# Kernel optimization log

Measured on AMD Instinct MI355X. Metric: run time of the kernel, lower is better.

Reference implementation:

```python
import jax, jax.numpy as jnp
import numpy as np

N, E, D_IN, H, D = 170000, 1200000, 128, 4, 32
NEG_SLOPE = 0.2


def setup_inputs() -> dict:
    key = jax.random.key(0)
    ks = jax.random.split(key, 8)
    x = jax.random.normal(ks[0], (N, D_IN), dtype=jnp.float32)
    # xavier-normal-ish scale for linear weights
    W_embed = jax.random.normal(ks[1], (D_IN, H * D), dtype=jnp.float32) * (2.0 / (D_IN + H * D)) ** 0.5
    a_src = jax.random.normal(ks[2], (H, D), dtype=jnp.float32) * (2.0 / (1 + H * D)) ** 0.5
    a_dst = jax.random.normal(ks[3], (H, D), dtype=jnp.float32) * (2.0 / (1 + H * D)) ** 0.5
    W_lin = jax.random.normal(ks[4], (D_IN, H * D), dtype=jnp.float32) * (2.0 / (D_IN + H * D)) ** 0.5
    bias = jnp.zeros((H * D,), dtype=jnp.float32)
    src = jax.random.randint(ks[5], (E,), 0, N, dtype=jnp.int32)
    dst = jax.random.randint(ks[6], (E,), 0, N, dtype=jnp.int32)
    return {"x": x, "W_embed": W_embed, "a_src": a_src, "a_dst": a_dst,
            "W_lin": W_lin, "bias": bias, "src": src, "dst": dst}


def reference(x, W_embed, a_src, a_dst, W_lin, bias, src, dst):
    n = x.shape[0]
    # node projections: [N, H, D]
    h = (x @ W_embed).reshape(n, H, D)
    dot_src = jnp.einsum('nhd,hd->nh', h, a_src)  # [N, H]
    dot_dst = jnp.einsum('nhd,hd->nh', h, a_dst)  # [N, H]
    # edge attention logits: leaky_relu(dot_src[u] + dot_dst[v])  [E, H]
    z = dot_src[src] + dot_dst[dst]
    logit = jnp.where(z >= 0, z, NEG_SLOPE * z)
    # edge softmax over incoming edges of each destination node
    m = jax.ops.segment_max(logit, dst, num_segments=n)          # [N, H]
    e = jnp.exp(logit - m[dst])                                   # [E, H]
    denom = jax.ops.segment_sum(e, dst, num_segments=n)          # [N, H]
    prob = e / denom[dst]                                         # [E, H]
    # weighted scatter-sum aggregation: sum_e prob_e * h[src_e]
    msg = h[src] * prob[:, :, None]                               # [E, H, D]
    out = jax.ops.segment_sum(msg, dst, num_segments=n)          # [N, H, D]
    out = out.reshape(n, H * D)
    out = out + x @ W_lin
    out = out + bias[None, :]
    return out
```

## Files before the change

kernel.cpp:

```cpp
#include <hip/hip_runtime.h>
#include <hip/hip_bf16.h>

static constexpr int   N_NODES   = 170000;
static constexpr int   E_EDGES   = 1200000;
static constexpr float NEG_SLOPE = 0.2f;

typedef __attribute__((ext_vector_type(8))) short bfrag8;
typedef __attribute__((ext_vector_type(4))) float facc4;

__device__ __forceinline__ short f2bf(float f) {
    __hip_bfloat16 h = __float2bfloat16(f);
    return *reinterpret_cast<short*>(&h);
}

__global__ void wt_init_kernel(const float* __restrict__ We,
                               const float* __restrict__ Wl,
                               const float* __restrict__ a_src,
                               const float* __restrict__ a_dst,
                               short* __restrict__ WtG,
                               int* __restrict__ deg)
{
    const int t = threadIdx.x;
    if (blockIdx.x < 128) {
        const int k = blockIdx.x;
        if (t < 128) WtG[t * 128 + k] = f2bf(We[k * 128 + t]);
        else         WtG[t * 128 + k] = f2bf(Wl[k * 128 + (t - 128)]);
    } else if (blockIdx.x < 136) {
        const int idx = (blockIdx.x - 128) * 256 + t;
        if (idx < 1024) {
            const int g = idx >> 7;
            const int k = idx & 127;
            const int hh = g & 3;
            const float* av = (g < 4) ? a_src : a_dst;
            float s = 0.f;
            #pragma unroll
            for (int d = 0; d < 32; ++d)
                s += We[k * 128 + hh * 32 + d] * av[hh * 32 + d];
            WtG[(256 + g) * 128 + k] = f2bf(s);
        } else {
            const int z = idx - 1024;
            WtG[(264 + (z >> 7)) * 128 + (z & 127)] = 0;
        }
    }
    const int i = blockIdx.x * 256 + t;
    if (i < N_NODES) deg[i] = 0;
}

__global__ void hist_kernel(const int* __restrict__ dst,
                            int* __restrict__ deg,
                            int* __restrict__ seq)
{
    int e = blockIdx.x * blockDim.x + threadIdx.x;
    if (e < E_EDGES) {
        const int s = atomicAdd(&deg[dst[e]], 1);
        __builtin_nontemporal_store(s, &seq[e]);
    }
}

__global__ __launch_bounds__(256) void scan_local_kernel(
    const int* __restrict__ deg, int* __restrict__ row_ptr, int* __restrict__ bsum)
{
    __shared__ int sh[256];
    const int t = threadIdx.x;
    const int base = blockIdx.x * 1024 + t * 4;
    int v0 = (base + 0 < N_NODES) ? deg[base + 0] : 0;
    int v1 = (base + 1 < N_NODES) ? deg[base + 1] : 0;
    int v2 = (base + 2 < N_NODES) ? deg[base + 2] : 0;
    int v3 = (base + 3 < N_NODES) ? deg[base + 3] : 0;
    const int tot = v0 + v1 + v2 + v3;
    sh[t] = tot;
    __syncthreads();
    for (int off = 1; off < 256; off <<= 1) {
        int add = (t >= off) ? sh[t - off] : 0;
        __syncthreads();
        sh[t] += add;
        __syncthreads();
    }
    const int excl = sh[t] - tot;
    if (base + 0 < N_NODES) row_ptr[base + 0] = excl;
    if (base + 1 < N_NODES) row_ptr[base + 1] = excl + v0;
    if (base + 2 < N_NODES) row_ptr[base + 2] = excl + v0 + v1;
    if (base + 3 < N_NODES) row_ptr[base + 3] = excl + v0 + v1 + v2;
    if (t == 255) bsum[blockIdx.x] = sh[255];
}

__global__ __launch_bounds__(256) void scan_block_kernel(
    const int* __restrict__ bsum, int* __restrict__ boff, int nblk)
{
    __shared__ int sh[256];
    const int t = threadIdx.x;
    const int v = (t < nblk) ? bsum[t] : 0;
    sh[t] = v;
    __syncthreads();
    for (int off = 1; off < 256; off <<= 1) {
        int add = (t >= off) ? sh[t - off] : 0;
        __syncthreads();
        sh[t] += add;
        __syncthreads();
    }
    boff[t] = sh[t] - v;
}

__global__ void scan_add_kernel(int* __restrict__ row_ptr,
                                const int* __restrict__ boff)
{
    int i = blockIdx.x * blockDim.x + threadIdx.x;
    if (i < N_NODES) row_ptr[i] += boff[i >> 10];
    if (i == 0) row_ptr[N_NODES] = E_EDGES;
}

__global__ void csr_place_kernel(const int* __restrict__ src,
                                 const int* __restrict__ dst,
                                 const int* __restrict__ seq,
                                 const int* __restrict__ rowp,
                                 int* __restrict__ srcs)
{
    int e = blockIdx.x * blockDim.x + threadIdx.x;
    if (e >= E_EDGES) return;
    const int p = rowp[dst[e]] + seq[e];
    __builtin_nontemporal_store(src[e], &srcs[p]);
}

static constexpr int LDB = 136;

__global__ __launch_bounds__(256, 2) void mfma_gemm_kernel(
    const float* __restrict__ x,
    const short* __restrict__ WtG,
    const float* __restrict__ bias,
    short* __restrict__ hbuf,
    float* __restrict__ dsrc,
    float* __restrict__ ddst,
    float* __restrict__ outp)
{
    __shared__ short Bs[272 * LDB];
    const int tid  = threadIdx.x;
    const long row0 = (long)blockIdx.x * 128;

    #pragma unroll
    for (int it = 0; it < 17; ++it) {
        const int idx = it * 256 + tid;
        const int n   = idx >> 4;
        const int kc  = (idx & 15) * 8;
        *(int4*)&Bs[n * LDB + kc] = *(const int4*)&WtG[n * 128 + kc];
    }

    const int w    = tid >> 6;
    const int l    = tid & 63;
    const int col  = l & 15;
    const int quad = l >> 4;

    long ar0 = row0 + w * 32 + col;
    long ar1 = ar0 + 16;
    if (ar0 > N_NODES - 1) ar0 = N_NODES - 1;
    if (ar1 > N_NODES - 1) ar1 = N_NODES - 1;
    const float4* xp0 = (const float4*)&x[ar0 * 128 + quad * 8];
    const float4* xp1 = (const float4*)&x[ar1 * 128 + quad * 8];
    float4 av[2][4][2];
    #pragma unroll
    for (int ks = 0; ks < 4; ++ks) {
        av[0][ks][0] = xp0[ks * 8 + 0];
        av[0][ks][1] = xp0[ks * 8 + 1];
        av[1][ks][0] = xp1[ks * 8 + 0];
        av[1][ks][1] = xp1[ks * 8 + 1];
    }
    bfrag8 afr[2][4];
    #pragma unroll
    for (int m = 0; m < 2; ++m)
        #pragma unroll
        for (int ks = 0; ks < 4; ++ks) {
            bfrag8 t;
            t[0] = f2bf(av[m][ks][0].x); t[1] = f2bf(av[m][ks][0].y);
            t[2] = f2bf(av[m][ks][0].z); t[3] = f2bf(av[m][ks][0].w);
            t[4] = f2bf(av[m][ks][1].x); t[5] = f2bf(av[m][ks][1].y);
            t[6] = f2bf(av[m][ks][1].z); t[7] = f2bf(av[m][ks][1].w);
            afr[m][ks] = t;
        }
    __syncthreads();

    facc4 acc[2][8];
    facc4 adot[2];

    #pragma unroll
    for (int m = 0; m < 2; ++m) {
        adot[m] = (facc4)(0.f);
        #pragma unroll
        for (int t = 0; t < 8; ++t) acc[m][t] = (facc4)(0.f);
    }

    #pragma unroll
    for (int ks = 0; ks < 4; ++ks) {
        #pragma unroll
        for (int t = 0; t < 8; ++t) {
            const bfrag8 b = *(const bfrag8*)&Bs[(t * 16 + col) * LDB + ks * 32 + quad * 8];
            acc[0][t] = __builtin_amdgcn_mfma_f32_16x16x32_bf16(afr[0][ks], b, acc[0][t], 0, 0, 0);
            acc[1][t] = __builtin_amdgcn_mfma_f32_16x16x32_bf16(afr[1][ks], b, acc[1][t], 0, 0, 0);
        }
        const bfrag8 bd = *(const bfrag8*)&Bs[(256 + col) * LDB + ks * 32 + quad * 8];
        adot[0] = __builtin_amdgcn_mfma_f32_16x16x32_bf16(afr[0][ks], bd, adot[0], 0, 0, 0);
        adot[1] = __builtin_amdgcn_mfma_f32_16x16x32_bf16(afr[1][ks], bd, adot[1], 0, 0, 0);
    }

    #pragma unroll
    for (int m = 0; m < 2; ++m) {
        const long rbase = row0 + w * 32 + m * 16 + quad * 4;
        #pragma unroll
        for (int r = 0; r < 4; ++r) {
            const long mm = rbase + r;
            if (mm >= N_NODES) continue;
            #pragma unroll
            for (int t = 0; t < 8; ++t)
                hbuf[mm * 128 + t * 16 + col] = f2bf(acc[m][t][r]);
            if (col < 4)      dsrc[mm * 4 + col]       = adot[m][r];
            else if (col < 8) ddst[mm * 4 + (col - 4)] = adot[m][r];
        }
    }

    #pragma unroll
    for (int m = 0; m < 2; ++m)
        #pragma unroll
        for (int t = 0; t < 8; ++t) acc[m][t] = (facc4)(0.f);

    #pragma unroll
    for (int ks = 0; ks < 4; ++ks) {
        #pragma unroll
        for (int t = 0; t < 8; ++t) {
            const bfrag8 b = *(const bfrag8*)&Bs[(128 + t * 16 + col) * LDB + ks * 32 + quad * 8];
            acc[0][t] = __builtin_amdgcn_mfma_f32_16x16x32_bf16(afr[0][ks], b, acc[0][t], 0, 0, 0);
            acc[1][t] = __builtin_amdgcn_mfma_f32_16x16x32_bf16(afr[1][ks], b, acc[1][t], 0, 0, 0);
        }
    }

    #pragma unroll
    for (int t = 0; t < 8; ++t) {
        const float bv = bias[t * 16 + col];
        #pragma unroll
        for (int m = 0; m < 2; ++m) {
            const long rbase = row0 + w * 32 + m * 16 + quad * 4;
            #pragma unroll
            for (int r = 0; r < 4; ++r) {
                const long mm = rbase + r;
                if (mm < N_NODES) outp[mm * 128 + t * 16 + col] = acc[m][t][r] + bv;
            }
        }
    }
}

__global__ __launch_bounds__(256) void agg_kernel(
    const int* __restrict__ row_ptr, const int* __restrict__ srcs,
    const float* __restrict__ dsrc, const float* __restrict__ ddst,
    const short* __restrict__ hbuf, float* __restrict__ outp)
{
    const long node = (long)blockIdx.x * 4 + (threadIdx.x >> 6);
    if (node >= N_NODES) return;
    const int lane = threadIdx.x & 63;
    const int head = lane >> 4;
    const int c2   = lane << 1;
    const int start = __builtin_amdgcn_readfirstlane(row_ptr[node]);
    const int end   = __builtin_amdgcn_readfirstlane(row_ptr[node + 1]);
    if (start == end) return;

    const float dd = ddst[node * 4 + head];

    float a0 = 0.f, a1 = 0.f, dn = 0.f;

#define EDGE_LOAD(i) \
    const int   s##i = __builtin_amdgcn_readlane(sv, k + i); \
    const float e##i = dsrc[s##i * 4 + head]; \
    const uint  h##i = *(const uint*)&hbuf[(long)s##i * 128 + c2];

#define EDGE_ACC(i) { \
    float z = e##i + dd; \
    z = (z >= 0.f) ? z : NEG_SLOPE * z; \
    float wv = __expf(z); \
    if (k + i >= chunk) wv = 0.f; \
    dn += wv; \
    a0 = fmaf(wv, __uint_as_float(h##i << 16),        a0); \
    a1 = fmaf(wv, __uint_as_float(h##i & 0xFFFF0000u), a1); }

    int j = start;
    while (j < end) {
        const int rem   = end - j;
        const int chunk = rem < 64 ? rem : 64;
        int idx = j + lane;
        if (idx > end - 1) idx = end - 1;
        const int sv = srcs[idx];
        for (int k = 0; k < chunk; k += 8) {
            EDGE_LOAD(0) EDGE_LOAD(1) EDGE_LOAD(2) EDGE_LOAD(3)
            EDGE_LOAD(4) EDGE_LOAD(5) EDGE_LOAD(6) EDGE_LOAD(7)
            EDGE_ACC(0) EDGE_ACC(1) EDGE_ACC(2) EDGE_ACC(3)
            EDGE_ACC(4) EDGE_ACC(5) EDGE_ACC(6) EDGE_ACC(7)
        }
        j += chunk;
    }
#undef EDGE_LOAD
#undef EDGE_ACC

    const float inv = 1.f / dn;
    float2* op = (float2*)&outp[node * 128 + c2];
    float2 o = *op;
    o.x += a0 * inv;
    o.y += a1 * inv;
    *op = o;
}

extern "C" void kernel_launch(void* const* d_in, const int* in_sizes, int n_in,
                              void* d_out, int out_size, void* d_ws, size_t ws_size,
                              hipStream_t stream)
{
    const float* x       = (const float*)d_in[0];
    const float* W_embed = (const float*)d_in[1];
    const float* a_src   = (const float*)d_in[2];
    const float* a_dst   = (const float*)d_in[3];
    const float* W_lin   = (const float*)d_in[4];
    const float* bias    = (const float*)d_in[5];
    const int*   src     = (const int*)d_in[6];
    const int*   dst     = (const int*)d_in[7];
    float* outp = (float*)d_out;

    char* ws = (char*)d_ws;
    short* WtG   = (short*)ws;  ws += (size_t)272 * 128 * sizeof(short);
    short* hbuf  = (short*)ws;  ws += (size_t)N_NODES * 128 * sizeof(short);
    int*   srcs  = (int*)ws;    ws += (size_t)E_EDGES * sizeof(int);
    float* dsrc  = (float*)ws;  ws += (size_t)N_NODES * 4 * sizeof(float);
    float* ddst  = (float*)ws;  ws += (size_t)N_NODES * 4 * sizeof(float);
    int*   deg   = (int*)ws;    ws += (size_t)N_NODES * sizeof(int);
    int*   rowp  = (int*)ws;    ws += (size_t)(N_NODES + 16) * sizeof(int);
    int*   bsum  = (int*)ws;    ws += 256 * sizeof(int);
    int*   boff  = (int*)ws;    ws += 256 * sizeof(int);

    int* seq = (int*)dsrc;

    const int SCAN_BLKS = (N_NODES + 1023) / 1024;

    wt_init_kernel<<<(N_NODES + 255) / 256, 256, 0, stream>>>(
        W_embed, W_lin, a_src, a_dst, WtG, deg);
    hist_kernel<<<(E_EDGES + 255) / 256, 256, 0, stream>>>(dst, deg, seq);
    scan_local_kernel<<<SCAN_BLKS, 256, 0, stream>>>(deg, rowp, bsum);
    scan_block_kernel<<<1, 256, 0, stream>>>(bsum, boff, SCAN_BLKS);
    scan_add_kernel<<<(N_NODES + 255) / 256, 256, 0, stream>>>(rowp, boff);

    csr_place_kernel<<<(E_EDGES + 255) / 256, 256, 0, stream>>>(
        src, dst, seq, rowp, srcs);

    mfma_gemm_kernel<<<(N_NODES + 127) / 128, 256, 0, stream>>>(
        x, WtG, bias, hbuf, dsrc, ddst, outp);

    agg_kernel<<<(N_NODES + 3) / 4, 256, 0, stream>>>(
        rowp, srcs, dsrc, ddst, hbuf, outp);
}
```

Before: 389.7 us.

## Halve GEMM LDS footprint with staged weight loads; precompute edge weights per lane in aggregation

```diff
diff --git a/kernel.cpp b/kernel.cpp
--- a/kernel.cpp
+++ b/kernel.cpp
@@ -123,7 +123,7 @@
 
 static constexpr int LDB = 136;
 
-__global__ __launch_bounds__(256, 2) void mfma_gemm_kernel(
+__global__ __launch_bounds__(256, 4) void mfma_gemm_kernel(
     const float* __restrict__ x,
     const short* __restrict__ WtG,
     const float* __restrict__ bias,
@@ -132,17 +132,9 @@
     float* __restrict__ ddst,
     float* __restrict__ outp)
 {
-    __shared__ short Bs[272 * LDB];
+    __shared__ short Bs[144 * LDB];
     const int tid  = threadIdx.x;
     const long row0 = (long)blockIdx.x * 128;
-
-    #pragma unroll
-    for (int it = 0; it < 17; ++it) {
-        const int idx = it * 256 + tid;
-        const int n   = idx >> 4;
-        const int kc  = (idx & 15) * 8;
-        *(int4*)&Bs[n * LDB + kc] = *(const int4*)&WtG[n * 128 + kc];
-    }
 
     const int w    = tid >> 6;
     const int l    = tid & 63;
@@ -163,6 +155,16 @@
         av[1][ks][0] = xp1[ks * 8 + 0];
         av[1][ks][1] = xp1[ks * 8 + 1];
     }
+
+    #pragma unroll
+    for (int it = 0; it < 9; ++it) {
+        const int idx = it * 256 + tid;
+        const int n   = idx >> 4;
+        const int kc  = (idx & 15) * 8;
+        const int gn  = (n < 128) ? n : (n + 128);
+        *(int4*)&Bs[n * LDB + kc] = *(const int4*)&WtG[gn * 128 + kc];
+    }
+
     bfrag8 afr[2][4];
     #pragma unroll
     for (int m = 0; m < 2; ++m)
@@ -195,7 +197,7 @@
             acc[0][t] = __builtin_amdgcn_mfma_f32_16x16x32_bf16(afr[0][ks], b, acc[0][t], 0, 0, 0);
             acc[1][t] = __builtin_amdgcn_mfma_f32_16x16x32_bf16(afr[1][ks], b, acc[1][t], 0, 0, 0);
         }
-        const bfrag8 bd = *(const bfrag8*)&Bs[(256 + col) * LDB + ks * 32 + quad * 8];
+        const bfrag8 bd = *(const bfrag8*)&Bs[(128 + col) * LDB + ks * 32 + quad * 8];
         adot[0] = __builtin_amdgcn_mfma_f32_16x16x32_bf16(afr[0][ks], bd, adot[0], 0, 0, 0);
         adot[1] = __builtin_amdgcn_mfma_f32_16x16x32_bf16(afr[1][ks], bd, adot[1], 0, 0, 0);
     }
@@ -215,6 +217,16 @@
         }
     }
 
+    __syncthreads();
+    #pragma unroll
+    for (int it = 0; it < 8; ++it) {
+        const int idx = it * 256 + tid;
+        const int n   = idx >> 4;
+        const int kc  = (idx & 15) * 8;
+        *(int4*)&Bs[n * LDB + kc] = *(const int4*)&WtG[(128 + n) * 128 + kc];
+    }
+    __syncthreads();
+
     #pragma unroll
     for (int m = 0; m < 2; ++m)
         #pragma unroll
@@ -224,7 +236,7 @@
     for (int ks = 0; ks < 4; ++ks) {
         #pragma unroll
         for (int t = 0; t < 8; ++t) {
-            const bfrag8 b = *(const bfrag8*)&Bs[(128 + t * 16 + col) * LDB + ks * 32 + quad * 8];
+            const bfrag8 b = *(const bfrag8*)&Bs[(t * 16 + col) * LDB + ks * 32 + quad * 8];
             acc[0][t] = __builtin_amdgcn_mfma_f32_16x16x32_bf16(afr[0][ks], b, acc[0][t], 0, 0, 0);
             acc[1][t] = __builtin_amdgcn_mfma_f32_16x16x32_bf16(afr[1][ks], b, acc[1][t], 0, 0, 0);
         }
@@ -252,47 +264,44 @@
 {
     const long node = (long)blockIdx.x * 4 + (threadIdx.x >> 6);
     if (node >= N_NODES) return;
-    const int lane = threadIdx.x & 63;
-    const int head = lane >> 4;
-    const int c2   = lane << 1;
+    const int lane   = threadIdx.x & 63;
+    const int head_c = lane >> 4;
+    const int c2     = lane << 1;
+    const int slot   = lane >> 2;
+    const int head_w = lane & 3;
     const int start = __builtin_amdgcn_readfirstlane(row_ptr[node]);
     const int end   = __builtin_amdgcn_readfirstlane(row_ptr[node + 1]);
     if (start == end) return;
 
-    const float dd = ddst[node * 4 + head];
+    const float ddw = ddst[node * 4 + head_w];
 
     float a0 = 0.f, a1 = 0.f, dn = 0.f;
 
-#define EDGE_LOAD(i) \
-    const int   s##i = __builtin_amdgcn_readlane(sv, k + i); \
-    const float e##i = dsrc[s##i * 4 + head]; \
+#define EDGE_BODY(i) \
+    const float w##i = __shfl(wv, (k + i) * 4 + head_c); \
+    const int   s##i = __builtin_amdgcn_readlane(sv, (k + i) * 4); \
     const uint  h##i = *(const uint*)&hbuf[(long)s##i * 128 + c2];
 
 #define EDGE_ACC(i) { \
-    float z = e##i + dd; \
-    z = (z >= 0.f) ? z : NEG_SLOPE * z; \
-    float wv = __expf(z); \
-    if (k + i >= chunk) wv = 0.f; \
-    dn += wv; \
-    a0 = fmaf(wv, __uint_as_float(h##i << 16),        a0); \
-    a1 = fmaf(wv, __uint_as_float(h##i & 0xFFFF0000u), a1); }
-
-    int j = start;
-    while (j < end) {
-        const int rem   = end - j;
-        const int chunk = rem < 64 ? rem : 64;
-        int idx = j + lane;
-        if (idx > end - 1) idx = end - 1;
-        const int sv = srcs[idx];
-        for (int k = 0; k < chunk; k += 8) {
-            EDGE_LOAD(0) EDGE_LOAD(1) EDGE_LOAD(2) EDGE_LOAD(3)
-            EDGE_LOAD(4) EDGE_LOAD(5) EDGE_LOAD(6) EDGE_LOAD(7)
+    dn += w##i; \
+    a0 = fmaf(w##i, __uint_as_float(h##i << 16),         a0); \
+    a1 = fmaf(w##i, __uint_as_float(h##i & 0xFFFF0000u), a1); }
+
+    for (int j = start; j < end; j += 16) {
+        const int idx = j + slot;
+        const int ci  = (idx < end) ? idx : (end - 1);
+        const int sv  = srcs[ci];
+        float z = dsrc[sv * 4 + head_w] + ddw;
+        z = fmaxf(z, NEG_SLOPE * z);
+        float wv = __expf(z);
+        if (idx >= end) wv = 0.f;
+        const int chunk = (end - j < 16) ? (end - j) : 16;
+        for (int k = 0; k < chunk; k += 4) {
+            EDGE_BODY(0) EDGE_BODY(1) EDGE_BODY(2) EDGE_BODY(3)
             EDGE_ACC(0) EDGE_ACC(1) EDGE_ACC(2) EDGE_ACC(3)
-            EDGE_ACC(4) EDGE_ACC(5) EDGE_ACC(6) EDGE_ACC(7)
-        }
-        j += chunk;
-    }
-#undef EDGE_LOAD
+        }
+    }
+#undef EDGE_BODY
 #undef EDGE_ACC
 
     const float inv = 1.f / dn;
```

Result: slower. 401.1 us (+2.9%).
